# Kernel optimization log

Measured on AMD Instinct MI355X. Metric: run time of the kernel, lower is better.

Reference implementation:

```python
import jax, jax.numpy as jnp
import numpy as np

B, T, E = 4, 2048, 2048
G, QG, D = 4, 4, 128  # kv groups, queries per group, head dim; H = G*QG = 16


def rope(x):
    # x: (..., T, D); rotate-half rotary positional embedding over the T axis
    t, d = x.shape[-2], x.shape[-1]
    half = d // 2
    inv_freq = 1.0 / (10000.0 ** (jnp.arange(half, dtype=jnp.float32) / half))
    ang = jnp.arange(t, dtype=jnp.float32)[:, None] * inv_freq[None, :]  # (T, half)
    cos, sin = jnp.cos(ang), jnp.sin(ang)
    x1, x2 = x[..., :half], x[..., half:]
    return jnp.concatenate([x1 * cos - x2 * sin, x1 * sin + x2 * cos], axis=-1)


def setup_inputs() -> dict:
    key = jax.random.key(0)
    ks = jax.random.split(key, 5)
    s = 0.02
    return {
        "x": jax.random.normal(ks[0], (B, T, E), dtype=jnp.float32),
        "Wq": jax.random.normal(ks[1], (E, G * QG * D), dtype=jnp.float32) * s,
        "Wk": jax.random.normal(ks[2], (E, G * D), dtype=jnp.float32) * s,
        "Wv": jax.random.normal(ks[3], (E, G * D), dtype=jnp.float32) * s,
        "Wo": jax.random.normal(ks[4], (G * QG * D, E), dtype=jnp.float32) * s,
    }


def reference(x, Wq, Wk, Wv, Wo):
    b, t, e = x.shape
    q = (x @ Wq).reshape(b, t, G, QG, D).transpose(0, 2, 3, 1, 4)  # (B,G,QG,T,D)
    k = (x @ Wk).reshape(b, t, G, D).transpose(0, 2, 1, 3)          # (B,G,T,D)
    v = (x @ Wv).reshape(b, t, G, D).transpose(0, 2, 1, 3)          # (B,G,T,D)
    q = rope(q)
    k = rope(k)
    scores = jnp.einsum("bgqtd,bgsd->bgqts", q, k) / jnp.sqrt(jnp.float32(D))
    causal = jnp.tril(jnp.ones((t, t), dtype=bool))                 # query t attends to s<=t
    scores = jnp.where(causal, scores, jnp.float32(-1e9))
    probs = jax.nn.softmax(scores, axis=-1)                         # (B,G,QG,T,T) explicit probs
    attn = jnp.einsum("bgqts,bgsd->bgqtd", probs, v)
    out = attn.transpose(0, 3, 1, 2, 4).reshape(b, t, G * QG * D)
    return out @ Wo
```

## Files before the change

kernel.cpp:

```cpp
#include <hip/hip_runtime.h>
#include <hip/hip_bf16.h>

typedef unsigned short u16;
typedef unsigned u32;
typedef float f32x4 __attribute__((ext_vector_type(4)));
typedef float f32x16 __attribute__((ext_vector_type(16)));
typedef short bf16x8 __attribute__((ext_vector_type(8)));

#define B_ 4
#define T_ 2048
#define E_ 2048
#define G_ 4
#define QG_ 4
#define D_ 128
#define H_ 16
#define BT_ 8192
#define SCALE2 0.12752745907f

__device__ __forceinline__ u16 f2bf(float f) {
  union { float f; unsigned u; } v; v.f = f;
  unsigned r = v.u + 0x7fffu + ((v.u >> 16) & 1u);
  return (u16)(r >> 16);
}
__device__ __forceinline__ float bf2f(u16 b) {
  union { unsigned u; float f; } v; v.u = ((unsigned)b) << 16;
  return v.f;
}
__device__ __forceinline__ unsigned packbf2(float lo, float hi) {
  __hip_bfloat162 h2 = __float22bfloat162_rn(make_float2(lo, hi));
  union { __hip_bfloat162 h; unsigned u; } cv; cv.h = h2; return cv.u;
}
#define EXP2F(x) __builtin_amdgcn_exp2f(x)

#define GL2LDS(g, l) __builtin_amdgcn_global_load_lds( \
    (const __attribute__((address_space(1))) void*)(g), \
    (__attribute__((address_space(3))) void*)(l), 16, 0, 0)

#define MFMA(a, b, c) __builtin_amdgcn_mfma_f32_16x16x32_bf16((a), (b), (c), 0, 0, 0)
#define MFMA32(a, b, c) __builtin_amdgcn_mfma_f32_32x32x16_bf16((a), (b), (c), 0, 0, 0)


__global__ void k_cvt_x(const float4* __restrict__ x, uint2* __restrict__ xb) {
  int i = blockIdx.x * 256 + threadIdx.x;
  float4 v = x[i];
  uint2 o;
  o.x = (unsigned)f2bf(v.x) | ((unsigned)f2bf(v.y) << 16);
  o.y = (unsigned)f2bf(v.z) | ((unsigned)f2bf(v.w) << 16);
  xb[i] = o;
}

__global__ void k_cvt_wT(const float* __restrict__ W, u16* __restrict__ WT,
                         int R, int C) {
  __shared__ float tile[64][65];
  int c0 = blockIdx.x * 64, r0 = blockIdx.y * 64;
  int tid = threadIdx.x;
#pragma unroll
  for (int p = 0; p < 16; ++p) {
    int idx = p * 256 + tid;
    int i = idx >> 6, j = idx & 63;
    tile[i][j] = W[(size_t)(r0 + i) * C + c0 + j];
  }
  __syncthreads();
#pragma unroll
  for (int p = 0; p < 16; ++p) {
    int idx = p * 256 + tid;
    int i = idx >> 6, j = idx & 63;
    WT[(size_t)(c0 + i) * R + r0 + j] = f2bf(tile[j][i]);
  }
}

__global__ void k_tables(float* __restrict__ ct, float* __restrict__ st) {
  int i = blockIdx.x * 256 + threadIdx.x;
  int t = i >> 6, j = i & 63;
  float freq = powf(10000.f, -(float)j / 64.f);
  float ang = (float)t * freq;
  ct[i] = cosf(ang);
  st[i] = sinf(ang);
}


template <int OUTBF>
__global__ __launch_bounds__(256) void k_gemm_bt(
    const u16* __restrict__ A, const u16* __restrict__ BT,
    void* __restrict__ C, int M, int N, int K) {
  __shared__ u16 As[128 * 32];
  __shared__ u16 Bs[128 * 32];
  const int tid = threadIdx.x;
  const int wave = tid >> 6;
  const int lane = tid & 63;
  const int lo = lane & 15, hi = lane >> 4;
  const int m0 = blockIdx.y * 128, n0 = blockIdx.x * 128;
  const int wm = (wave >> 1) * 64, wn = (wave & 1) * 64;
  f32x4 acc[4][4] = {};

  for (int k0 = 0; k0 < K; k0 += 32) {
#pragma unroll
    for (int r = 0; r < 2; ++r) {
      int c = r * 256 + tid;
      int row = c >> 2, kc = c & 3;
      GL2LDS(A + (size_t)(m0 + row) * K + k0 + kc * 8,
             &As[(r * 256 + wave * 64) * 8]);
      GL2LDS(BT + (size_t)(n0 + row) * K + k0 + kc * 8,
             &Bs[(r * 256 + wave * 64) * 8]);
    }
    __syncthreads();
    bf16x8 af[4], bfr[4];
#pragma unroll
    for (int i = 0; i < 4; ++i) {
      af[i]  = *(const bf16x8*)&As[(wm + i * 16 + lo) * 32 + hi * 8];
      bfr[i] = *(const bf16x8*)&Bs[(wn + i * 16 + lo) * 32 + hi * 8];
    }
#pragma unroll
    for (int i = 0; i < 4; ++i)
#pragma unroll
      for (int j = 0; j < 4; ++j)
        acc[i][j] = MFMA(af[i], bfr[j], acc[i][j]);
    __syncthreads();
  }
#pragma unroll
  for (int i = 0; i < 4; ++i)
#pragma unroll
    for (int j = 0; j < 4; ++j)
#pragma unroll
      for (int r = 0; r < 4; ++r) {
        int row = m0 + wm + i * 16 + hi * 4 + r;
        int col = n0 + wn + j * 16 + lo;
        if (OUTBF) ((u16*)C)[(size_t)row * N + col] = f2bf(acc[i][j][r]);
        else       ((float*)C)[(size_t)row * N + col] = acc[i][j][r];
      }
}


__device__ __forceinline__ void rd_frag(bf16x8* dst, const u16* Xs,
                                        int r0, int r1, int r2, int r3,
                                        int lo, int hi) {
  int rows[4] = {r0, r1, r2, r3};
#pragma unroll
  for (int i = 0; i < 4; ++i) {
    int rw = rows[i] + lo;
    dst[i] = *(const bf16x8*)&Xs[(rw >> 1) * 64 +
        (((((rw & 1) << 2) | hi)) ^ ((rw >> 1) & 7)) * 8];
  }
}
__device__ __forceinline__ void mm16(f32x4 (*acc)[4], const bf16x8* a,
                                     const bf16x8* b) {
#pragma unroll
  for (int i = 0; i < 4; ++i)
#pragma unroll
    for (int j = 0; j < 4; ++j)
      acc[i][j] = MFMA(a[i], b[j], acc[i][j]);
}

template <int MODE>
__global__ __launch_bounds__(512, 2) void k_gemm256(
    const u16* __restrict__ A, const u16* __restrict__ Bt,
    void* __restrict__ C, const float* __restrict__ ct,
    const float* __restrict__ st, int M, int N, int K) {
  __shared__ u16 As[4][8192];
  __shared__ u16 Bs[4][8192];
  const int tid = threadIdx.x;
  const int wave = tid >> 6, lane = tid & 63;
  const int lo = lane & 15, hi = lane >> 4;
  const int nbn = N >> 8;
  const int bn = blockIdx.x % nbn;
  const int bm = blockIdx.x / nbn;
  const int m0 = bm * 256, n0 = bn * 256;
  const int wm = wave >> 2, wn = wave & 3;
  const int bbase = (MODE == 2) ? ((wn & 1) * 32 + (wn >> 1) * 128) : wn * 64;
  const int BO2 = (MODE == 2) ? 64 : 32;
  const int BO3 = (MODE == 2) ? 80 : 48;

  f32x4 acc[8][4] = {};

  auto stage = [&](const u16* __restrict__ X, int x0, u16* dstBase, int kcol) {
#pragma unroll
    for (int r = 0; r < 2; ++r) {
      int idx = r * 512 + tid;
      int pair = idx >> 3;
      int u = (idx & 7) ^ (pair & 7);
      GL2LDS(X + (size_t)(x0 + pair * 2 + (u >> 2)) * K + kcol + (u & 3) * 8,
             dstBase + (r * 512 + wave * 64) * 8);
    }
  };

  const int NT = K >> 6;
  stage(A, m0, &As[0][0], 0);
  stage(Bt, n0, &Bs[0][0], 0);
  stage(A, m0, &As[1][0], 32);
  stage(Bt, n0, &Bs[1][0], 32);
  asm volatile("s_waitcnt vmcnt(4)" ::: "memory");
  __builtin_amdgcn_s_barrier();

  for (int t = 0; t < NT; ++t) {
    const int s0 = (t & 1) << 1;
    const int sn = s0 ^ 2;
    const bool pf = (t + 1 < NT);
    const int kc = (t + 1) << 6;

    bf16x8 b0[4], b1[4], a[4];
    rd_frag(b0, &Bs[s0][0], bbase, bbase + 16, bbase + BO2, bbase + BO3, lo, hi);
    rd_frag(a, &As[s0][0], wm * 128, wm * 128 + 16, wm * 128 + 32, wm * 128 + 48, lo, hi);
    if (pf) stage(A, m0, &As[sn][0], kc);
    __builtin_amdgcn_s_barrier();
    __builtin_amdgcn_s_setprio(1);
    mm16(&acc[0], a, b0);
    __builtin_amdgcn_s_setprio(0);
    __builtin_amdgcn_s_barrier();
    rd_frag(a, &As[s0][0], wm * 128 + 64, wm * 128 + 80, wm * 128 + 96, wm * 128 + 112, lo, hi);
    if (pf) {
      stage(Bt, n0, &Bs[sn][0], kc);
      asm volatile("s_waitcnt vmcnt(4)" ::: "memory");
    } else {
      asm volatile("s_waitcnt vmcnt(0)" ::: "memory");
    }
    __builtin_amdgcn_s_barrier();
    __builtin_amdgcn_s_setprio(1);
    mm16(&acc[4], a, b0);
    __builtin_amdgcn_s_setprio(0);
    __builtin_amdgcn_s_barrier();
    rd_frag(b1, &Bs[s0 + 1][0], bbase, bbase + 16, bbase + BO2, bbase + BO3, lo, hi);
    rd_frag(a, &As[s0 + 1][0], wm * 128, wm * 128 + 16, wm * 128 + 32, wm * 128 + 48, lo, hi);
    if (pf) stage(A, m0, &As[sn + 1][0], kc + 32);
    __builtin_amdgcn_s_barrier();
    __builtin_amdgcn_s_setprio(1);
    mm16(&acc[0], a, b1);
    __builtin_amdgcn_s_setprio(0);
    __builtin_amdgcn_s_barrier();
    rd_frag(a, &As[s0 + 1][0], wm * 128 + 64, wm * 128 + 80, wm * 128 + 96, wm * 128 + 112, lo, hi);
    if (pf) {
      stage(Bt, n0, &Bs[sn + 1][0], kc + 32);
      asm volatile("s_waitcnt vmcnt(4)" ::: "memory");
    }
    __builtin_amdgcn_s_barrier();
    __builtin_amdgcn_s_setprio(1);
    mm16(&acc[4], a, b1);
    __builtin_amdgcn_s_setprio(0);
    __builtin_amdgcn_s_barrier();
  }

  if (MODE == 2) {
    const int hh = (n0 >> 7) + (wn >> 1);
    u16* qout = (u16*)C;
#pragma unroll
    for (int i = 0; i < 8; ++i)
#pragma unroll
      for (int r = 0; r < 4; ++r) {
        int rr = m0 + wm * 128 + i * 16 + hi * 4 + r;
        int bb = rr >> 11, tt = rr & (T_ - 1);
        size_t ro = ((size_t)((bb << 4) + hh) * T_ + tt) * (size_t)D_;
#pragma unroll
        for (int j = 0; j < 2; ++j) {
          int d1 = (wn & 1) * 32 + j * 16 + lo;
          float c = ct[tt * 64 + d1], s = st[tt * 64 + d1];
          float x1 = acc[i][j][r], x2 = acc[i][j + 2][r];
          qout[ro + d1]      = f2bf((x1 * c - x2 * s) * SCALE2);
          qout[ro + d1 + 64] = f2bf((x1 * s + x2 * c) * SCALE2);
        }
      }
  } else {
#pragma unroll
    for (int i = 0; i < 8; ++i)
#pragma unroll
      for (int j = 0; j < 4; ++j)
#pragma unroll
        for (int r = 0; r < 4; ++r) {
          int row = m0 + wm * 128 + i * 16 + hi * 4 + r;
          int col = n0 + wn * 64 + j * 16 + lo;
          ((float*)C)[(size_t)row * N + col] = acc[i][j][r];
        }
  }
}


__global__ void k_rope(const u16* __restrict__ src, u16* __restrict__ dst,
                       const float* __restrict__ ct, const float* __restrict__ st,
                       int sstr) {
  int i = blockIdx.x * 256 + threadIdx.x;
  int j = i & 63;
  int h = (i >> 6) & 3;
  int bt = i >> 8;
  int t = bt & (T_ - 1), b = bt >> 11;
  size_t srow = (size_t)bt * sstr + (size_t)h * D_;
  float x1 = bf2f(src[srow + j]);
  float x2 = bf2f(src[srow + 64 + j]);
  float c = ct[t * 64 + j], s = st[t * 64 + j];
  size_t drow = (((size_t)((b << 2) + h)) * T_ + t) << 7;
  dst[drow + j]      = f2bf(x1 * c - x2 * s);
  dst[drow + 64 + j] = f2bf(x1 * s + x2 * c);
}

__global__ void k_vtrans(const u16* __restrict__ vg, u16* __restrict__ vT,
                         int sstr) {
  __shared__ u16 tile[64][65];
  int t0 = blockIdx.x * 64;
  int d0 = blockIdx.y * 64;
  int bg = blockIdx.z;
  int g = bg & (G_ - 1), b = bg >> 2;
  int tid = threadIdx.x;
#pragma unroll
  for (int p = 0; p < 16; ++p) {
    int idx = p * 256 + tid;
    int i = idx >> 6, j = idx & 63;
    tile[i][j] = vg[(size_t)(b * T_ + t0 + i) * sstr + g * D_ + d0 + j];
  }
  __syncthreads();
#pragma unroll
  for (int p = 0; p < 16; ++p) {
    int idx = p * 256 + tid;
    int i = idx >> 6, j = idx & 63;
    vT[((size_t)bg * D_ + d0 + i) * T_ + t0 + j] = tile[j][i];
  }
}


__device__ __forceinline__ void swap32(u32 a, u32 b, u32& x, u32& y) {
#if __has_builtin(__builtin_amdgcn_permlane32_swap)
  auto rr = __builtin_amdgcn_permlane32_swap(a, b, false, false);
  x = rr[0]; y = rr[1];
#else
  u32 as = __shfl_xor(a, 32), bs = __shfl_xor(b, 32);
  int hi = (threadIdx.x & 63) >> 5;
  x = hi ? bs : a;
  y = hi ? b : as;
#endif
}

__global__ __launch_bounds__(256, 2) void k_attn(
    const u16* __restrict__ qh, const u16* __restrict__ kh,
    const u16* __restrict__ vT, u16* __restrict__ ab) {
  __shared__ u16 Ks[2][64 * 128];
  __shared__ u16 Vs[2][128 * 64];
  const int tid = threadIdx.x;
  const int wave = tid >> 6;
  const int lane = tid & 63;
  const int l5 = lane & 31, h1 = lane >> 5;

  const int f = blockIdx.x;
  const int xcd = f & 7;
  const int slot = f >> 3;
  const int bg = xcd * 2 + (slot & 1);
  const int rest = slot >> 1;
  const int qg = rest & 3;
  const int i0 = (15 - (rest >> 2)) * 128;
  const int b = bg >> 2, g = bg & 3;
  const int h = g * 4 + qg;
  const int bh = b * 16 + h;

  const int qw0 = i0 + wave * 32;
  const int q = qw0 + l5;

  const u16* Qrow = qh + ((size_t)bh * T_ + q) * D_;
  bf16x8 qf[8];
#pragma unroll
  for (int kk = 0; kk < 8; ++kk)
    qf[kk] = *(const bf16x8*)(Qrow + kk * 16 + h1 * 8);

  const u16* Kbase = kh + (size_t)(b * G_ + g) * T_ * D_;
  const u16* Vbase = vT + (size_t)(b * G_ + g) * D_ * T_;

  auto stage = [&](int bi, int s0) {
#pragma unroll
    for (int r = 0; r < 4; ++r) {
      int p = r * 256 + tid;
      {
        int row = p >> 4, c = p & 15;
        GL2LDS(Kbase + (size_t)(s0 + row) * D_ + ((c ^ (row & 7)) * 8),
               &Ks[bi][(r * 256 + wave * 64) * 8]);
      }
      {
        int row = p >> 3, c = p & 7;
        GL2LDS(Vbase + (size_t)row * T_ + s0 + ((c ^ (row & 7)) * 8),
               &Vs[bi][(r * 256 + wave * 64) * 8]);
      }
    }
  };

  f32x16 acc[4] = {};
  float mrun = -1e30f, lrun = 0.f;

  const int nt = ((i0 + 127) >> 6) + 1;
  stage(0, 0);
  int bufc = 0;
  for (int ti = 0; ti < nt; ++ti) {
    const int s0 = ti << 6;
    __syncthreads();
    if (ti + 1 < nt) stage(bufc ^ 1, (ti + 1) << 6);
    if (s0 <= qw0 + 31) {
      f32x16 sa[2] = {};
#pragma unroll
      for (int st = 0; st < 2; ++st) {
        if (s0 + st * 32 <= qw0 + 31) {
#pragma unroll
          for (int kk = 0; kk < 8; ++kk) {
            int row = st * 32 + l5;
            bf16x8 kf = *(const bf16x8*)
                &Ks[bufc][row * 128 + ((2 * kk + h1) ^ (row & 7)) * 8];
            sa[st] = MFMA32(kf, qf[kk], sa[st]);
          }
        }
      }
#pragma unroll
      for (int st = 0; st < 2; ++st) {
        const bool needm = (s0 + st * 32 + 31 > qw0);
        if (needm) {
#pragma unroll
          for (int r = 0; r < 16; ++r) {
            int s = s0 + st * 32 + (r & 3) + 8 * (r >> 2) + 4 * h1;
            if (s > q) sa[st][r] = -1e9f;
          }
        }
      }
      float mx[16];
#pragma unroll
      for (int r = 0; r < 16; ++r) mx[r] = fmaxf(sa[0][r], sa[1][r]);
#pragma unroll
      for (int off = 8; off >= 1; off >>= 1)
#pragma unroll
        for (int r = 0; r < 8; ++r)
          if (r < off) mx[r] = fmaxf(mx[r], mx[r + off]);
      float pm = fmaxf(mx[0], __shfl_xor(mx[0], 32));
      if (!__all(pm - mrun <= 8.f)) {
        float mn = fmaxf(mrun, pm);
        float alpha = EXP2F(mrun - mn);
#pragma unroll
        for (int dt = 0; dt < 4; ++dt)
#pragma unroll
          for (int r = 0; r < 16; ++r) acc[dt][r] *= alpha;
        lrun *= alpha;
        mrun = mn;
      }
      bf16x8 pf[4];
      float se[16];
#pragma unroll
      for (int st = 0; st < 2; ++st) {
        float pe[16];
#pragma unroll
        for (int r = 0; r < 16; ++r) {
          pe[r] = EXP2F(sa[st][r] - mrun);
          if (st == 0) se[r] = pe[r]; else se[r] += pe[r];
        }
#pragma unroll
        for (int kl = 0; kl < 2; ++kl) {
          u32 w0 = packbf2(pe[kl * 8 + 0], pe[kl * 8 + 1]);
          u32 w1 = packbf2(pe[kl * 8 + 2], pe[kl * 8 + 3]);
          u32 y0 = packbf2(pe[kl * 8 + 4], pe[kl * 8 + 5]);
          u32 y1 = packbf2(pe[kl * 8 + 6], pe[kl * 8 + 7]);
          union { u32 w[4]; bf16x8 v; } pw;
          swap32(w0, y0, pw.w[0], pw.w[2]);
          swap32(w1, y1, pw.w[1], pw.w[3]);
          pf[st * 2 + kl] = pw.v;
        }
      }
#pragma unroll
      for (int off = 8; off >= 1; off >>= 1)
#pragma unroll
        for (int r = 0; r < 8; ++r)
          if (r < off) se[r] += se[r + off];
      lrun += se[0] + __shfl_xor(se[0], 32);
#pragma unroll
      for (int ks = 0; ks < 4; ++ks) {
#pragma unroll
        for (int dt = 0; dt < 4; ++dt) {
          int row = dt * 32 + l5;
          bf16x8 vf = *(const bf16x8*)
              &Vs[bufc][row * 64 + ((2 * ks + h1) ^ (row & 7)) * 8];
          acc[dt] = MFMA32(vf, pf[ks], acc[dt]);
        }
      }
    }
    bufc ^= 1;
  }
  const float iv = 1.f / lrun;
  u16* outrow = ab + ((size_t)(b * T_ + q)) * (H_ * D_) + (size_t)h * D_;
#pragma unroll
  for (int dt = 0; dt < 4; ++dt)
#pragma unroll
    for (int g4 = 0; g4 < 4; ++g4) {
      uint2 o;
      o.x = (u32)f2bf(acc[dt][g4 * 4 + 0] * iv) |
            ((u32)f2bf(acc[dt][g4 * 4 + 1] * iv) << 16);
      o.y = (u32)f2bf(acc[dt][g4 * 4 + 2] * iv) |
            ((u32)f2bf(acc[dt][g4 * 4 + 3] * iv) << 16);
      *(uint2*)(outrow + dt * 32 + 8 * g4 + 4 * h1) = o;
    }
}


extern "C" void kernel_launch(void* const* d_in, const int* in_sizes, int n_in,
                              void* d_out, int out_size, void* d_ws, size_t ws_size,
                              hipStream_t stream) {
  const float* x  = (const float*)d_in[0];
  const float* Wq = (const float*)d_in[1];
  const float* Wk = (const float*)d_in[2];
  const float* Wv = (const float*)d_in[3];
  const float* Wo = (const float*)d_in[4];

  char* base = (char*)d_ws;
  size_t off = 0;
  auto nxt = [&](size_t bytes) {
    char* r = base + off;
    off += (bytes + 255) & ~(size_t)255;
    return r;
  };
  u16*   xb  = (u16*)nxt((size_t)BT_ * E_ * 2);
  u16*   wqT = (u16*)nxt((size_t)E_ * E_ * 2);
  u16*   kvT = (u16*)nxt((size_t)1024 * E_ * 2);
  u16*   woT = (u16*)nxt((size_t)E_ * E_ * 2);
  float* ct  = (float*)nxt((size_t)T_ * 64 * 4);
  float* st  = (float*)nxt((size_t)T_ * 64 * 4);
  u16*   qhb = (u16*)nxt((size_t)BT_ * E_ * 2);
  u16*   kvg = (u16*)nxt((size_t)BT_ * 1024 * 2);
  u16*   vTb = (u16*)nxt((size_t)BT_ * (G_ * D_) * 2);
  u16* khb = wqT;
  u16* ab  = xb;

  k_cvt_x<<<BT_ * E_ / 4 / 256, 256, 0, stream>>>((const float4*)x, (uint2*)xb);
  k_cvt_wT<<<dim3(E_ / 64, E_ / 64), 256, 0, stream>>>(Wq, wqT, E_, E_);
  k_cvt_wT<<<dim3((G_ * D_) / 64, E_ / 64), 256, 0, stream>>>(Wk, kvT, E_, G_ * D_);
  k_cvt_wT<<<dim3((G_ * D_) / 64, E_ / 64), 256, 0, stream>>>(
      Wv, kvT + (size_t)(G_ * D_) * E_, E_, G_ * D_);
  k_cvt_wT<<<dim3(E_ / 64, E_ / 64), 256, 0, stream>>>(Wo, woT, E_, E_);
  k_tables<<<T_ * 64 / 256, 256, 0, stream>>>(ct, st);

  k_gemm256<2><<<dim3((E_ / 256) * (BT_ / 256)), 512, 0, stream>>>(
      xb, wqT, qhb, ct, st, BT_, E_, E_);
  k_gemm_bt<1><<<dim3(1024 / 128, BT_ / 128), 256, 0, stream>>>(
      xb, kvT, kvg, BT_, 1024, E_);

  k_rope<<<BT_ * G_ * 64 / 256, 256, 0, stream>>>(kvg, khb, ct, st, 1024);
  k_vtrans<<<dim3(T_ / 64, D_ / 64, B_ * G_), 256, 0, stream>>>(
      kvg + G_ * D_, vTb, 1024);

  k_attn<<<dim3(1024), 256, 0, stream>>>(qhb, khb, vTb, ab);

  k_gemm256<0><<<dim3((E_ / 256) * (BT_ / 256)), 512, 0, stream>>>(
      ab, woT, d_out, nullptr, nullptr, BT_, E_, E_);
}
```

Before: 341.9 us.

## Fuse Q, K, V projections into one GEMM with in-epilogue RoPE

Concatenates the transposed Wq, Wk and Wv weights into a single 3072-column matrix and computes Q, K and V with one pipelined 256x256 GEMM launch instead of a separate Q GEMM plus a smaller K/V GEMM. RoPE for K is applied in the epilogue, which removes the standalone rope kernel and its extra read and write pass. V tiles are written as plain bf16 for the existing transpose kernel. This cuts launches and the round trip of K through memory, at the cost of a branchier epilogue and a separate K buffer no longer aliased onto the weight workspace.

Result: faster. 326.5 us (-4.5%).

```diff
diff --git a/kernel.cpp b/kernel.cpp
--- a/kernel.cpp
+++ b/kernel.cpp
@@ -79,58 +79,6 @@
 }
 
 
-template <int OUTBF>
-__global__ __launch_bounds__(256) void k_gemm_bt(
-    const u16* __restrict__ A, const u16* __restrict__ BT,
-    void* __restrict__ C, int M, int N, int K) {
-  __shared__ u16 As[128 * 32];
-  __shared__ u16 Bs[128 * 32];
-  const int tid = threadIdx.x;
-  const int wave = tid >> 6;
-  const int lane = tid & 63;
-  const int lo = lane & 15, hi = lane >> 4;
-  const int m0 = blockIdx.y * 128, n0 = blockIdx.x * 128;
-  const int wm = (wave >> 1) * 64, wn = (wave & 1) * 64;
-  f32x4 acc[4][4] = {};
-
-  for (int k0 = 0; k0 < K; k0 += 32) {
-#pragma unroll
-    for (int r = 0; r < 2; ++r) {
-      int c = r * 256 + tid;
-      int row = c >> 2, kc = c & 3;
-      GL2LDS(A + (size_t)(m0 + row) * K + k0 + kc * 8,
-             &As[(r * 256 + wave * 64) * 8]);
-      GL2LDS(BT + (size_t)(n0 + row) * K + k0 + kc * 8,
-             &Bs[(r * 256 + wave * 64) * 8]);
-    }
-    __syncthreads();
-    bf16x8 af[4], bfr[4];
-#pragma unroll
-    for (int i = 0; i < 4; ++i) {
-      af[i]  = *(const bf16x8*)&As[(wm + i * 16 + lo) * 32 + hi * 8];
-      bfr[i] = *(const bf16x8*)&Bs[(wn + i * 16 + lo) * 32 + hi * 8];
-    }
-#pragma unroll
-    for (int i = 0; i < 4; ++i)
-#pragma unroll
-      for (int j = 0; j < 4; ++j)
-        acc[i][j] = MFMA(af[i], bfr[j], acc[i][j]);
-    __syncthreads();
-  }
-#pragma unroll
-  for (int i = 0; i < 4; ++i)
-#pragma unroll
-    for (int j = 0; j < 4; ++j)
-#pragma unroll
-      for (int r = 0; r < 4; ++r) {
-        int row = m0 + wm + i * 16 + hi * 4 + r;
-        int col = n0 + wn + j * 16 + lo;
-        if (OUTBF) ((u16*)C)[(size_t)row * N + col] = f2bf(acc[i][j][r]);
-        else       ((float*)C)[(size_t)row * N + col] = acc[i][j][r];
-      }
-}
-
-
 __device__ __forceinline__ void rd_frag(bf16x8* dst, const u16* Xs,
                                         int r0, int r1, int r2, int r3,
                                         int lo, int hi) {
@@ -155,7 +103,8 @@
 __global__ __launch_bounds__(512, 2) void k_gemm256(
     const u16* __restrict__ A, const u16* __restrict__ Bt,
     void* __restrict__ C, const float* __restrict__ ct,
-    const float* __restrict__ st, int M, int N, int K) {
+    const float* __restrict__ st, u16* __restrict__ kout,
+    u16* __restrict__ vout, int M, int N, int K) {
   __shared__ u16 As[4][8192];
   __shared__ u16 Bs[4][8192];
   const int tid = threadIdx.x;
@@ -166,9 +115,9 @@
   const int bm = blockIdx.x / nbn;
   const int m0 = bm * 256, n0 = bn * 256;
   const int wm = wave >> 2, wn = wave & 3;
-  const int bbase = (MODE == 2) ? ((wn & 1) * 32 + (wn >> 1) * 128) : wn * 64;
-  const int BO2 = (MODE == 2) ? 64 : 32;
-  const int BO3 = (MODE == 2) ? 80 : 48;
+  const int bbase = (MODE == 3) ? ((wn & 1) * 32 + (wn >> 1) * 128) : wn * 64;
+  const int BO2 = (MODE == 3) ? 64 : 32;
+  const int BO3 = (MODE == 3) ? 80 : 48;
 
   f32x4 acc[8][4] = {};
 
@@ -238,25 +187,42 @@
     __builtin_amdgcn_s_barrier();
   }
 
-  if (MODE == 2) {
-    const int hh = (n0 >> 7) + (wn >> 1);
-    u16* qout = (u16*)C;
-#pragma unroll
-    for (int i = 0; i < 8; ++i)
-#pragma unroll
-      for (int r = 0; r < 4; ++r) {
-        int rr = m0 + wm * 128 + i * 16 + hi * 4 + r;
-        int bb = rr >> 11, tt = rr & (T_ - 1);
-        size_t ro = ((size_t)((bb << 4) + hh) * T_ + tt) * (size_t)D_;
-#pragma unroll
-        for (int j = 0; j < 2; ++j) {
-          int d1 = (wn & 1) * 32 + j * 16 + lo;
-          float c = ct[tt * 64 + d1], s = st[tt * 64 + d1];
-          float x1 = acc[i][j][r], x2 = acc[i][j + 2][r];
-          qout[ro + d1]      = f2bf((x1 * c - x2 * s) * SCALE2);
-          qout[ro + d1 + 64] = f2bf((x1 * s + x2 * c) * SCALE2);
-        }
-      }
+  if (MODE == 3) {
+    if (bn >= 10) {
+      const int n0v = n0 - 2560;
+#pragma unroll
+      for (int i = 0; i < 8; ++i)
+#pragma unroll
+        for (int j = 0; j < 4; ++j)
+#pragma unroll
+          for (int r = 0; r < 4; ++r) {
+            int row = m0 + wm * 128 + i * 16 + hi * 4 + r;
+            int col = n0v + bbase + (j & 1) * 16 + (j >> 1) * 64 + lo;
+            vout[(size_t)row * 512 + col] = f2bf(acc[i][j][r]);
+          }
+    } else {
+      const bool isq = (bn < 8);
+      u16* out = isq ? (u16*)C : kout;
+      const int hh = (isq ? (n0 >> 7) : ((n0 - 2048) >> 7)) + (wn >> 1);
+      const int hbits = isq ? 4 : 2;
+      const float sc = isq ? SCALE2 : 1.0f;
+#pragma unroll
+      for (int i = 0; i < 8; ++i)
+#pragma unroll
+        for (int r = 0; r < 4; ++r) {
+          int rr = m0 + wm * 128 + i * 16 + hi * 4 + r;
+          int bb = rr >> 11, tt = rr & (T_ - 1);
+          size_t ro = ((size_t)((bb << hbits) + hh) * T_ + tt) << 7;
+#pragma unroll
+          for (int j = 0; j < 2; ++j) {
+            int d1 = (wn & 1) * 32 + j * 16 + lo;
+            float c = ct[tt * 64 + d1], s = st[tt * 64 + d1];
+            float x1 = acc[i][j][r], x2 = acc[i][j + 2][r];
+            out[ro + d1]      = f2bf((x1 * c - x2 * s) * sc);
+            out[ro + d1 + 64] = f2bf((x1 * s + x2 * c) * sc);
+          }
+        }
+    }
   } else {
 #pragma unroll
     for (int i = 0; i < 8; ++i)
@@ -269,24 +235,6 @@
           ((float*)C)[(size_t)row * N + col] = acc[i][j][r];
         }
   }
-}
-
-
-__global__ void k_rope(const u16* __restrict__ src, u16* __restrict__ dst,
-                       const float* __restrict__ ct, const float* __restrict__ st,
-                       int sstr) {
-  int i = blockIdx.x * 256 + threadIdx.x;
-  int j = i & 63;
-  int h = (i >> 6) & 3;
-  int bt = i >> 8;
-  int t = bt & (T_ - 1), b = bt >> 11;
-  size_t srow = (size_t)bt * sstr + (size_t)h * D_;
-  float x1 = bf2f(src[srow + j]);
-  float x2 = bf2f(src[srow + 64 + j]);
-  float c = ct[t * 64 + j], s = st[t * 64 + j];
-  size_t drow = (((size_t)((b << 2) + h)) * T_ + t) << 7;
-  dst[drow + j]      = f2bf(x1 * c - x2 * s);
-  dst[drow + 64 + j] = f2bf(x1 * s + x2 * c);
 }
 
 __global__ void k_vtrans(const u16* __restrict__ vg, u16* __restrict__ vT,
@@ -502,37 +450,33 @@
     off += (bytes + 255) & ~(size_t)255;
     return r;
   };
-  u16*   xb  = (u16*)nxt((size_t)BT_ * E_ * 2);
-  u16*   wqT = (u16*)nxt((size_t)E_ * E_ * 2);
-  u16*   kvT = (u16*)nxt((size_t)1024 * E_ * 2);
-  u16*   woT = (u16*)nxt((size_t)E_ * E_ * 2);
-  float* ct  = (float*)nxt((size_t)T_ * 64 * 4);
-  float* st  = (float*)nxt((size_t)T_ * 64 * 4);
-  u16*   qhb = (u16*)nxt((size_t)BT_ * E_ * 2);
-  u16*   kvg = (u16*)nxt((size_t)BT_ * 1024 * 2);
-  u16*   vTb = (u16*)nxt((size_t)BT_ * (G_ * D_) * 2);
-  u16* khb = wqT;
-  u16* ab  = xb;
+  u16*   xb   = (u16*)nxt((size_t)BT_ * E_ * 2);
+  u16*   wAll = (u16*)nxt((size_t)3072 * E_ * 2);
+  u16*   woT  = (u16*)nxt((size_t)E_ * E_ * 2);
+  float* ct   = (float*)nxt((size_t)T_ * 64 * 4);
+  float* st   = (float*)nxt((size_t)T_ * 64 * 4);
+  u16*   qhb  = (u16*)nxt((size_t)BT_ * E_ * 2);
+  u16*   khb  = (u16*)nxt((size_t)BT_ * (G_ * D_) * 2);
+  u16*   vg   = (u16*)nxt((size_t)BT_ * (G_ * D_) * 2);
+  u16*   vTb  = (u16*)nxt((size_t)BT_ * (G_ * D_) * 2);
+  u16* ab = xb;
 
   k_cvt_x<<<BT_ * E_ / 4 / 256, 256, 0, stream>>>((const float4*)x, (uint2*)xb);
-  k_cvt_wT<<<dim3(E_ / 64, E_ / 64), 256, 0, stream>>>(Wq, wqT, E_, E_);
-  k_cvt_wT<<<dim3((G_ * D_) / 64, E_ / 64), 256, 0, stream>>>(Wk, kvT, E_, G_ * D_);
+  k_cvt_wT<<<dim3(E_ / 64, E_ / 64), 256, 0, stream>>>(Wq, wAll, E_, E_);
   k_cvt_wT<<<dim3((G_ * D_) / 64, E_ / 64), 256, 0, stream>>>(
-      Wv, kvT + (size_t)(G_ * D_) * E_, E_, G_ * D_);
+      Wk, wAll + (size_t)2048 * E_, E_, G_ * D_);
+  k_cvt_wT<<<dim3((G_ * D_) / 64, E_ / 64), 256, 0, stream>>>(
+      Wv, wAll + (size_t)2560 * E_, E_, G_ * D_);
   k_cvt_wT<<<dim3(E_ / 64, E_ / 64), 256, 0, stream>>>(Wo, woT, E_, E_);
   k_tables<<<T_ * 64 / 256, 256, 0, stream>>>(ct, st);
 
-  k_gemm256<2><<<dim3((E_ / 256) * (BT_ / 256)), 512, 0, stream>>>(
-      xb, wqT, qhb, ct, st, BT_, E_, E_);
-  k_gemm_bt<1><<<dim3(1024 / 128, BT_ / 128), 256, 0, stream>>>(
-      xb, kvT, kvg, BT_, 1024, E_);
-
-  k_rope<<<BT_ * G_ * 64 / 256, 256, 0, stream>>>(kvg, khb, ct, st, 1024);
-  k_vtrans<<<dim3(T_ / 64, D_ / 64, B_ * G_), 256, 0, stream>>>(
-      kvg + G_ * D_, vTb, 1024);
+  k_gemm256<3><<<dim3((3072 / 256) * (BT_ / 256)), 512, 0, stream>>>(
+      xb, wAll, qhb, ct, st, khb, vg, BT_, 3072, E_);
+
+  k_vtrans<<<dim3(T_ / 64, D_ / 64, B_ * G_), 256, 0, stream>>>(vg, vTb, 512);
 
   k_attn<<<dim3(1024), 256, 0, stream>>>(qhb, khb, vTb, ab);
 
   k_gemm256<0><<<dim3((E_ / 256) * (BT_ / 256)), 512, 0, stream>>>(
-      ab, woT, d_out, nullptr, nullptr, BT_, E_, E_);
-}
+      ab, woT, d_out, nullptr, nullptr, nullptr, nullptr, BT_, E_, E_);
+}
```
